# Performance work log

Measured on AMD Instinct MI355X. Metric: run time of the kernel, lower is better.

## Reference

```python
import jax, jax.numpy as jnp
import numpy as np

B, IMG, P, D, E, K, H = 32, 224, 16, 512, 8, 2, 8
G = IMG // P
T = G * G          # 196 patches
PD = P * P         # 256 patch dim
FF = 4 * D         # expert hidden

def _posenc(t, d):
    pos = jnp.arange(t, dtype=jnp.float32)[:, None]
    i = jnp.arange(0, d, 2, dtype=jnp.float32)
    ang = pos / jnp.power(10000.0, i / d)
    pe = jnp.zeros((t, d), jnp.float32)
    pe = pe.at[:, 0::2].set(jnp.sin(ang))
    pe = pe.at[:, 1::2].set(jnp.cos(ang))
    return pe

def _attn(x, Wq, Wk, Wv, Wo, bo):
    bs, t, d = x.shape
    hs = d // H
    q = (x @ Wq).reshape(bs, t, H, hs).transpose(0, 2, 1, 3)
    k = (x @ Wk).reshape(bs, t, H, hs).transpose(0, 2, 1, 3)
    v = (x @ Wv).reshape(bs, t, H, hs).transpose(0, 2, 1, 3)
    wei = jnp.einsum('bhqd,bhkd->bhqk', q, k) * (hs ** -0.5)
    mask = jnp.tril(jnp.ones((t, t), dtype=bool))
    wei = jax.nn.softmax(jnp.where(mask, wei, -jnp.inf), axis=-1)
    o = jnp.einsum('bhqk,bhkd->bhqd', wei, v).transpose(0, 2, 1, 3).reshape(bs, t, d)
    return o @ Wo + bo

def _router(x, Wt, bt, Wn, bn, noise):
    # NoisyTopkRouter: noisy logits, top-k scatter to -inf background, softmax
    logits = x @ Wt + bt
    noisy = logits + noise * jax.nn.softplus(x @ Wn + bn)
    _, topi = jax.lax.top_k(noisy, K)
    sel = jax.nn.one_hot(topi, E, dtype=jnp.float32).sum(-2) > 0  # [B,T,E] bool
    return jax.nn.softmax(jnp.where(sel, noisy, -jnp.inf), axis=-1)

def _moe(x, gate, Wi, bi, Wo, bo):
    # gate is exactly zero off the top-k set, so dense all-expert compute
    # weighted by gate equals the original masked gather/scatter-add combine.
    h = jax.nn.relu(jnp.einsum('btd,edh->bteh', x, Wi) + bi)
    y = jnp.einsum('bteh,ehd->bted', h, Wo) + bo
    return jnp.einsum('bte,bted->btd', gate, y)

def _ln(x, g, b):
    mu = x.mean(-1, keepdims=True)
    var = ((x - mu) ** 2).mean(-1, keepdims=True)
    return (x - mu) / jnp.sqrt(var + 1e-5) * g + b

def _moe_layer(x, pW, pb, Wq, Wk, Wv, Wo, bo, rtW, rtb, rnW, rnb, eWi, ebi, eWo, ebo, lng, lnb, noise):
    x = x @ pW + pb                       # input_projection
    x = _attn(x, Wq, Wk, Wv, Wo, bo)      # multi-head causal self-attention
    gate = _router(x, rtW, rtb, rnW, rnb, noise)
    y = _moe(x, gate, eWi, ebi, eWo, ebo)
    return _ln(y, lng, lnb)               # dropout is identity in eval

def setup_inputs():
    key = jax.random.key(0)
    shapes = {"x": (B, 1, IMG, IMG), "pemb_W": (PD, D), "pemb_b": (D,), "vec_W": (D, D), "vec_b": (D,), "cls_W": (D, D), "cls_b": (D,)}
    for l in ("1", "2"):
        shapes.update({f"p{l}_W": (D, D), f"p{l}_b": (D,), f"Wq{l}": (D, D), f"Wk{l}": (D, D), f"Wv{l}": (D, D), f"Wo{l}": (D, D), f"bo{l}": (D,), f"rt{l}_W": (D, E), f"rt{l}_b": (E,), f"rn{l}_W": (D, E), f"rn{l}_b": (E,), f"eWi{l}": (E, D, FF), f"ebi{l}": (E, FF), f"eWo{l}": (E, FF, D), f"ebo{l}": (E, D), f"ln{l}_g": (D,), f"ln{l}_b": (D,), f"noise{l}": (B, T, E)})
    out = {}
    for i, (name, shp) in enumerate(shapes.items()):
        k = jax.random.fold_in(key, i)
        if name.startswith("ln") and name.endswith("_g"):
            out[name] = jnp.ones(shp, jnp.float32)
        else:
            scale = 1.0 if name == "x" or name.startswith("noise") else 0.02
            out[name] = jax.random.normal(k, shp, jnp.float32) * scale
    return out

def reference(x, pemb_W, pemb_b, vec_W, vec_b, cls_W, cls_b, p1_W, p1_b, Wq1, Wk1, Wv1, Wo1, bo1, rt1_W, rt1_b, rn1_W, rn1_b, eWi1, ebi1, eWo1, ebo1, ln1_g, ln1_b, noise1, p2_W, p2_b, Wq2, Wk2, Wv2, Wo2, bo2, rt2_W, rt2_b, rn2_W, rn2_b, eWi2, ebi2, eWo2, ebo2, ln2_g, ln2_b, noise2):
    bs = x.shape[0]
    # patchify (c==1): [B,1,IMG,IMG] -> [B,T,PD]
    patches = x[:, 0].reshape(bs, G, P, G, P).transpose(0, 1, 3, 2, 4).reshape(bs, T, PD)
    h = patches @ pemb_W + pemb_b + _posenc(T, D)[None]
    f1 = _moe_layer(h, p1_W, p1_b, Wq1, Wk1, Wv1, Wo1, bo1, rt1_W, rt1_b, rn1_W, rn1_b, eWi1, ebi1, eWo1, ebo1, ln1_g, ln1_b, noise1)
    first_vector = f1 @ vec_W + vec_b
    f2 = _moe_layer(first_vector, p2_W, p2_b, Wq2, Wk2, Wv2, Wo2, bo2, rt2_W, rt2_b, rn2_W, rn2_b, eWi2, ebi2, eWo2, ebo2, ln2_g, ln2_b, noise2)
    second_vector = f2 @ vec_W + vec_b
    # source bug: second_attn_weights is None; treated as uniform ones ->
    # mean over dim1 of ones is 1, so global = sum over patches.
    global_vector = second_vector.sum(axis=1)
    cls_vector = global_vector @ cls_W + cls_b
    return first_vector, second_vector, global_vector, cls_vector
```

## Files before the change

### kernel.cpp

```cpp
#include <hip/hip_runtime.h>

#define BT 6272
#define TT 196
#define DM 512
#define FFD 2048
#define NE 8
#define ABUF 3211264
#define SLOTS 12544

typedef float f32x4 __attribute__((ext_vector_type(4)));
typedef __bf16 bf16x8 __attribute__((ext_vector_type(8)));

__device__ __forceinline__ ushort f2bf(float f){
  union { float f; unsigned u; } v; v.f = f;
  unsigned u = v.u;
  u += 0x7fffu + ((u >> 16) & 1u);
  return (ushort)(u >> 16);
}
__device__ __forceinline__ float bf2f(ushort u){
  union { unsigned u; float f; } c; c.u = ((unsigned)u) << 16; return c.f;
}
__device__ __forceinline__ void splitbf(float v, ushort& hi, ushort& lo){
  union { float f; unsigned u; } c; c.f = v;
  hi = (ushort)(c.u >> 16);
  union { unsigned u; float f; } hf; hf.u = c.u & 0xffff0000u;
  lo = f2bf(v - hf.f);
}
__device__ __forceinline__ void glds16(const ushort* g, ushort* l){
  __builtin_amdgcn_global_load_lds(
      (const __attribute__((address_space(1))) unsigned int*)g,
      (__attribute__((address_space(3))) unsigned int*)l, 16, 0, 0);
}

__global__ void patchify_k(const float* __restrict__ x, ushort* __restrict__ oh, ushort* __restrict__ ol){
  int bt = blockIdx.x;
  int t = bt % TT, b = bt / TT;
  int pd = threadIdx.x;
  int g1 = t / 14, g2 = t % 14, p1 = pd >> 4, p2 = pd & 15;
  int src = (b*224 + g1*16 + p1)*224 + g2*16 + p2;
  float v = x[src];
  ushort hu, lu; splitbf(v, hu, lu);
  oh[(size_t)bt*256 + pd] = hu;
  ol[(size_t)bt*256 + pd] = lu;
}

__global__ void posenc_k(float* __restrict__ pe){
  int t = blockIdx.x, c = threadIdx.x;
  int m2 = c & ~1;
  double ang = (double)t * pow(10000.0, -(double)m2 / 512.0);
  double vv = (c & 1) ? cos(ang) : sin(ang);
  pe[t*DM + c] = (float)vv;
}

__global__ __launch_bounds__(256)
void wsplit_k(const float* __restrict__ src, ushort* __restrict__ dh, ushort* __restrict__ dl,
              int R, int C){
  __shared__ float t[32][33];
  int c0 = blockIdx.x << 5, r0 = blockIdx.y << 5;
  int tx = threadIdx.x & 31, ty = threadIdx.x >> 5;
  #pragma unroll
  for (int i = 0; i < 32; i += 8)
    t[ty+i][tx] = src[(size_t)(r0+ty+i)*C + c0 + tx];
  __syncthreads();
  #pragma unroll
  for (int i = 0; i < 32; i += 8){
    float v = t[tx][ty+i];
    ushort hu, lu; splitbf(v, hu, lu);
    dh[(size_t)(c0+ty+i)*R + r0 + tx] = hu;
    dl[(size_t)(c0+ty+i)*R + r0 + tx] = lu;
  }
}

__global__ __launch_bounds__(256)
void wsplit4_k(const float* __restrict__ s0, const float* __restrict__ s1,
               const float* __restrict__ s2, const float* __restrict__ s3,
               ushort* __restrict__ dQkvH, ushort* __restrict__ dQkvL,
               ushort* __restrict__ dWoH, ushort* __restrict__ dWoL)
{
  int z = blockIdx.z;
  const float* src = (z==0)? s0 : (z==1)? s1 : (z==2)? s2 : s3;
  ushort* dh; ushort* dl;
  if (z == 3){ dh = dWoH; dl = dWoL; }
  else { dh = dQkvH + (size_t)z*DM*DM; dl = dQkvL + (size_t)z*DM*DM; }
  __shared__ float t[32][33];
  int c0 = blockIdx.x << 5, r0 = blockIdx.y << 5;
  int tx = threadIdx.x & 31, ty = threadIdx.x >> 5;
  #pragma unroll
  for (int i = 0; i < 32; i += 8)
    t[ty+i][tx] = src[(size_t)(r0+ty+i)*DM + c0 + tx];
  __syncthreads();
  #pragma unroll
  for (int i = 0; i < 32; i += 8){
    float v = t[tx][ty+i];
    ushort hu, lu; splitbf(v, hu, lu);
    dh[(size_t)(c0+ty+i)*DM + r0 + tx] = hu;
    dl[(size_t)(c0+ty+i)*DM + r0 + tx] = lu;
  }
}

__global__ void esplit_k(const float* __restrict__ src, ushort* __restrict__ dh, ushort* __restrict__ dl){
  int i = blockIdx.x*256 + threadIdx.x;
  ushort hu, lu; splitbf(src[i], hu, lu);
  dh[i] = hu; dl[i] = lu;
}

__global__ __launch_bounds__(256)
void bfold_k(const float* __restrict__ pb, const float* __restrict__ Wq,
             const float* __restrict__ Wk, const float* __restrict__ Wv,
             float* __restrict__ bf){
  __shared__ float pbs[DM];
  int tid = threadIdx.x;
  for (int i = tid; i < DM; i += 256) pbs[i] = pb[i];
  __syncthreads();
  int n = blockIdx.x*256 + tid;
  const float* W = (n < 512) ? Wq : (n < 1024) ? Wk : Wv;
  int c = n & 511;
  float s = 0.f;
  for (int d = 0; d < DM; ++d) s += pbs[d] * W[(size_t)d*DM + c];
  bf[n] = s;
}

__global__ __launch_bounds__(256)
void gemm_s(const ushort* __restrict__ Ah, const ushort* __restrict__ Al,
            const ushort* __restrict__ Bh, const ushort* __restrict__ Bl,
            const float* __restrict__ bias, const float* __restrict__ pe,
            float* __restrict__ Cf, ushort* __restrict__ Ch, ushort* __restrict__ Cl,
            int N, int kld)
{
  __shared__ ushort Ahs[128*32];
  __shared__ ushort Als[128*32];
  __shared__ ushort Bhs[128*32];
  __shared__ ushort Bls[128*32];
  int tid = threadIdx.x;
  int row0 = blockIdx.y << 7, col0 = blockIdx.x << 7;
  int lane = tid & 63, w = tid >> 6;
  int wr = w >> 1, wc = w & 1;
  int fr = lane & 15, fu = lane >> 4;
  int srow = 16*w + (lane >> 2);
  int cs = ((lane & 3) ^ ((srow >> 1) & 3)) << 3;
  const ushort* gAh0 = Ah + (size_t)(row0 + srow) * kld + cs;
  const ushort* gAh1 = Ah + (size_t)(row0 + 64 + srow) * kld + cs;
  const ushort* gAl0 = Al + (size_t)(row0 + srow) * kld + cs;
  const ushort* gAl1 = Al + (size_t)(row0 + 64 + srow) * kld + cs;
  const ushort* gBh0 = Bh + (size_t)(col0 + srow) * kld + cs;
  const ushort* gBh1 = Bh + (size_t)(col0 + 64 + srow) * kld + cs;
  const ushort* gBl0 = Bl + (size_t)(col0 + srow) * kld + cs;
  const ushort* gBl1 = Bl + (size_t)(col0 + 64 + srow) * kld + cs;
  ushort* lAh0 = &Ahs[(16*w)*32];      ushort* lAh1 = &Ahs[(64+16*w)*32];
  ushort* lAl0 = &Als[(16*w)*32];      ushort* lAl1 = &Als[(64+16*w)*32];
  ushort* lBh0 = &Bhs[(16*w)*32];      ushort* lBh1 = &Bhs[(64+16*w)*32];
  ushort* lBl0 = &Bls[(16*w)*32];      ushort* lBl1 = &Bls[(64+16*w)*32];
  f32x4 acc[4][4] = {};
  for (int k0 = 0; k0 < kld; k0 += 32){
    __syncthreads();
    glds16(gAh0 + k0, lAh0); glds16(gAh1 + k0, lAh1);
    glds16(gAl0 + k0, lAl0); glds16(gAl1 + k0, lAl1);
    glds16(gBh0 + k0, lBh0); glds16(gBh1 + k0, lBh1);
    glds16(gBl0 + k0, lBl0); glds16(gBl1 + k0, lBl1);
    __syncthreads();
    bf16x8 ah[4], al[4];
    #pragma unroll
    for (int i = 0; i < 4; ++i){
      int Ra = (wr<<6) + (i<<4) + fr;
      int oa = Ra*32 + ((fu ^ ((Ra>>1)&3))<<3);
      ah[i] = *(const bf16x8*)&Ahs[oa];
      al[i] = *(const bf16x8*)&Als[oa];
    }
    #pragma unroll
    for (int j = 0; j < 4; ++j){
      int Rb = (wc<<6) + (j<<4) + fr;
      int ob = Rb*32 + ((fu ^ ((Rb>>1)&3))<<3);
      bf16x8 bh = *(const bf16x8*)&Bhs[ob];
      bf16x8 bl = *(const bf16x8*)&Bls[ob];
      #pragma unroll
      for (int i = 0; i < 4; ++i){
        acc[i][j] = __builtin_amdgcn_mfma_f32_16x16x32_bf16(ah[i], bh, acc[i][j], 0, 0, 0);
        acc[i][j] = __builtin_amdgcn_mfma_f32_16x16x32_bf16(al[i], bh, acc[i][j], 0, 0, 0);
        acc[i][j] = __builtin_amdgcn_mfma_f32_16x16x32_bf16(ah[i], bl, acc[i][j], 0, 0, 0);
      }
    }
  }
  int fq = lane >> 4;
  #pragma unroll
  for (int j = 0; j < 4; ++j){
    int col = col0 + (wc<<6) + (j<<4) + fr;
    float bv = bias ? bias[col] : 0.f;
    #pragma unroll
    for (int i = 0; i < 4; ++i){
      #pragma unroll
      for (int q = 0; q < 4; ++q){
        int rr = row0 + (wr<<6) + (i<<4) + (fq<<2) + q;
        float v = acc[i][j][q] + bv;
        if (pe) v += pe[(size_t)(rr % TT)*DM + col];
        size_t off = (size_t)rr*N + col;
        if (Cf) Cf[off] = v;
        if (Ch){
          ushort hu, lu; splitbf(v, hu, lu);
          Ch[off] = hu; Cl[off] = lu;
        }
      }
    }
  }
}

__global__ __launch_bounds__(256)
void gemm_f32(const float* __restrict__ A, const float* __restrict__ Bw,
              float* __restrict__ C, const float* __restrict__ bias,
              float* __restrict__ obf, int M, int N, int K)
{
  __shared__ float As[16][68];
  __shared__ float Bs[16][68];
  int tid = threadIdx.x;
  int row0 = blockIdx.y << 6, col0 = blockIdx.x << 6;
  int ar = tid >> 2, ak = (tid & 3) << 2;
  int bk = tid >> 4, bn = (tid & 15) << 2;
  int n0 = (tid & 15) << 2, m0 = (tid >> 4) << 2;
  float acc[4][4] = {};
  bool arow_ok = (row0 + ar) < M;
  const float* Aldg = A + (size_t)(row0 + ar) * K + ak;
  const float* Bldg = Bw + (size_t)bk * N + col0 + bn;
  for (int k0 = 0; k0 < K; k0 += 16){
    float4 av = make_float4(0.f,0.f,0.f,0.f);
    if (arow_ok) av = *(const float4*)(Aldg + k0);
    float4 bv = *(const float4*)(Bldg + (size_t)k0 * N);
    __syncthreads();
    As[ak+0][ar]=av.x; As[ak+1][ar]=av.y; As[ak+2][ar]=av.z; As[ak+3][ar]=av.w;
    *(float4*)&Bs[bk][bn] = bv;
    __syncthreads();
    #pragma unroll
    for (int kk = 0; kk < 16; ++kk){
      float4 a = *(const float4*)&As[kk][m0];
      float4 b = *(const float4*)&Bs[kk][n0];
      float aa[4] = {a.x,a.y,a.z,a.w};
      float bb[4] = {b.x,b.y,b.z,b.w};
      #pragma unroll
      for (int i = 0; i < 4; ++i)
        #pragma unroll
        for (int j = 0; j < 4; ++j)
          acc[i][j] += aa[i]*bb[j];
    }
  }
  float4 badd = make_float4(0.f,0.f,0.f,0.f);
  if (bias) badd = *(const float4*)(bias + col0 + n0);
  #pragma unroll
  for (int i = 0; i < 4; ++i){
    int gr = row0 + m0 + i;
    if (gr < M){
      float4 r = make_float4(acc[i][0]+badd.x, acc[i][1]+badd.y, acc[i][2]+badd.z, acc[i][3]+badd.w);
      *(float4*)(C + (size_t)gr*N + col0 + n0) = r;
      if (obf) *(float4*)(obf + (size_t)gr*N + col0 + n0) = r;
    }
  }
}

__global__ __launch_bounds__(256)
void fattn_k(const ushort* __restrict__ Xh, const ushort* __restrict__ Xl,
             ushort* __restrict__ oh, ushort* __restrict__ ol)
{
  __shared__ ushort Kh[64][72], Kl[64][72];
  __shared__ ushort Vth[64][72], Vtl[64][72];
  __shared__ ushort Ph[64][72], Pl[64][72];
  int qt = blockIdx.x, bh = blockIdx.y;
  int b = bh >> 3, h = bh & 7;
  int tid = threadIdx.x;
  int w = tid >> 6, lane = tid & 63;
  int fr = lane & 15, fu = lane >> 4;
  int qrow_f = qt*64 + w*16 + fr;
  int qtok = b*TT + (qrow_f < TT ? qrow_f : TT-1);
  const ushort* qph = Xh + (size_t)qtok*1536 + h*64 + fu*8;
  const ushort* qpl = Xl + (size_t)qtok*1536 + h*64 + fu*8;
  bf16x8 qh0 = *(const bf16x8*)(qph);
  bf16x8 qh1 = *(const bf16x8*)(qph + 32);
  bf16x8 ql0 = *(const bf16x8*)(qpl);
  bf16x8 ql1 = *(const bf16x8*)(qpl + 32);
  f32x4 o_acc[4] = {};
  float m_i[4], l_i[4];
  #pragma unroll
  for (int q = 0; q < 4; ++q){ m_i[q] = -3e38f; l_i[q] = 0.f; }
  int sr = tid >> 2, sc = (tid & 3) << 4;
  int ktiles = qt + 1;
  for (int kt = 0; kt < ktiles; ++kt){
    __syncthreads();
    {
      int jrow = kt*64 + sr;
      int jtok = b*TT + (jrow < TT ? jrow : TT-1);
      const ushort* kph = Xh + (size_t)jtok*1536 + 512 + h*64 + sc;
      const ushort* kpl = Xl + (size_t)jtok*1536 + 512 + h*64 + sc;
      *(uint4*)&Kh[sr][sc]   = *(const uint4*)kph;
      *(uint4*)&Kh[sr][sc+8] = *(const uint4*)(kph + 8);
      *(uint4*)&Kl[sr][sc]   = *(const uint4*)kpl;
      *(uint4*)&Kl[sr][sc+8] = *(const uint4*)(kpl + 8);
      const ushort* vph = Xh + (size_t)jtok*1536 + 1024 + h*64 + sc;
      const ushort* vpl = Xl + (size_t)jtok*1536 + 1024 + h*64 + sc;
      ushort tv[16];
      *(uint4*)&tv[0] = *(const uint4*)vph;
      *(uint4*)&tv[8] = *(const uint4*)(vph + 8);
      #pragma unroll
      for (int t = 0; t < 16; ++t) Vth[sc + t][sr] = tv[t];
      *(uint4*)&tv[0] = *(const uint4*)vpl;
      *(uint4*)&tv[8] = *(const uint4*)(vpl + 8);
      #pragma unroll
      for (int t = 0; t < 16; ++t) Vtl[sc + t][sr] = tv[t];
    }
    __syncthreads();
    f32x4 sacc[4] = {};
    #pragma unroll
    for (int j = 0; j < 4; ++j){
      bf16x8 kh0 = *(const bf16x8*)&Kh[j*16 + fr][fu*8];
      bf16x8 kh1 = *(const bf16x8*)&Kh[j*16 + fr][32 + fu*8];
      bf16x8 kl0 = *(const bf16x8*)&Kl[j*16 + fr][fu*8];
      bf16x8 kl1 = *(const bf16x8*)&Kl[j*16 + fr][32 + fu*8];
      sacc[j] = __builtin_amdgcn_mfma_f32_16x16x32_bf16(qh0, kh0, sacc[j], 0, 0, 0);
      sacc[j] = __builtin_amdgcn_mfma_f32_16x16x32_bf16(ql0, kh0, sacc[j], 0, 0, 0);
      sacc[j] = __builtin_amdgcn_mfma_f32_16x16x32_bf16(qh0, kl0, sacc[j], 0, 0, 0);
      sacc[j] = __builtin_amdgcn_mfma_f32_16x16x32_bf16(qh1, kh1, sacc[j], 0, 0, 0);
      sacc[j] = __builtin_amdgcn_mfma_f32_16x16x32_bf16(ql1, kh1, sacc[j], 0, 0, 0);
      sacc[j] = __builtin_amdgcn_mfma_f32_16x16x32_bf16(qh1, kl1, sacc[j], 0, 0, 0);
    }
    int rbase = qt*64 + w*16 + (fu<<2);
    int cg = kt*64 + fr;
    float p[4][4];
    #pragma unroll
    for (int q = 0; q < 4; ++q){
      int rg = rbase + q;
      float sv[4];
      #pragma unroll
      for (int j = 0; j < 4; ++j){
        int cj = cg + j*16;
        sv[j] = (cj <= rg && cj < TT) ? sacc[j][q]*0.125f : -3e38f;
      }
      float mx = fmaxf(fmaxf(sv[0],sv[1]), fmaxf(sv[2],sv[3]));
      #pragma unroll
      for (int off = 1; off < 16; off <<= 1) mx = fmaxf(mx, __shfl_xor(mx, off, 64));
      float mnew = fmaxf(m_i[q], mx);
      float al = expf(m_i[q] - mnew);
      l_i[q] *= al;
      o_acc[0][q] *= al; o_acc[1][q] *= al; o_acc[2][q] *= al; o_acc[3][q] *= al;
      float ps = 0.f;
      #pragma unroll
      for (int j = 0; j < 4; ++j){ p[q][j] = expf(sv[j] - mnew); ps += p[q][j]; }
      #pragma unroll
      for (int off = 1; off < 16; off <<= 1) ps += __shfl_xor(ps, off, 64);
      l_i[q] += ps;
      m_i[q] = mnew;
    }
    #pragma unroll
    for (int q = 0; q < 4; ++q){
      int pr = w*16 + (fu<<2) + q;
      #pragma unroll
      for (int j = 0; j < 4; ++j){
        ushort hu, lu; splitbf(p[q][j], hu, lu);
        Ph[pr][j*16 + fr] = hu;
        Pl[pr][j*16 + fr] = lu;
      }
    }
    bf16x8 ph0 = *(const bf16x8*)&Ph[w*16 + fr][fu*8];
    bf16x8 ph1 = *(const bf16x8*)&Ph[w*16 + fr][32 + fu*8];
    bf16x8 pl0 = *(const bf16x8*)&Pl[w*16 + fr][fu*8];
    bf16x8 pl1 = *(const bf16x8*)&Pl[w*16 + fr][32 + fu*8];
    #pragma unroll
    for (int jd = 0; jd < 4; ++jd){
      bf16x8 vh0 = *(const bf16x8*)&Vth[jd*16 + fr][fu*8];
      bf16x8 vh1 = *(const bf16x8*)&Vth[jd*16 + fr][32 + fu*8];
      bf16x8 vl0 = *(const bf16x8*)&Vtl[jd*16 + fr][fu*8];
      bf16x8 vl1 = *(const bf16x8*)&Vtl[jd*16 + fr][32 + fu*8];
      o_acc[jd] = __builtin_amdgcn_mfma_f32_16x16x32_bf16(ph0, vh0, o_acc[jd], 0, 0, 0);
      o_acc[jd] = __builtin_amdgcn_mfma_f32_16x16x32_bf16(pl0, vh0, o_acc[jd], 0, 0, 0);
      o_acc[jd] = __builtin_amdgcn_mfma_f32_16x16x32_bf16(ph0, vl0, o_acc[jd], 0, 0, 0);
      o_acc[jd] = __builtin_amdgcn_mfma_f32_16x16x32_bf16(ph1, vh1, o_acc[jd], 0, 0, 0);
      o_acc[jd] = __builtin_amdgcn_mfma_f32_16x16x32_bf16(pl1, vh1, o_acc[jd], 0, 0, 0);
      o_acc[jd] = __builtin_amdgcn_mfma_f32_16x16x32_bf16(ph1, vl1, o_acc[jd], 0, 0, 0);
    }
  }
  #pragma unroll
  for (int q = 0; q < 4; ++q){
    int rg = qt*64 + w*16 + (fu<<2) + q;
    if (rg < TT){
      float inv = 1.f / l_i[q];
      size_t rowoff = (size_t)(b*TT + rg)*DM + h*64 + fr;
      #pragma unroll
      for (int jd = 0; jd < 4; ++jd){
        float v = o_acc[jd][q] * inv;
        ushort hu, lu; splitbf(v, hu, lu);
        oh[rowoff + jd*16] = hu;
        ol[rowoff + jd*16] = lu;
      }
    }
  }
}

__global__ __launch_bounds__(256)
void router2_k(const ushort* __restrict__ Xh, const ushort* __restrict__ Xl,
               const float* __restrict__ rtW, const float* __restrict__ rtb,
               const float* __restrict__ rnW, const float* __restrict__ rnb, const float* __restrict__ nz,
               int* __restrict__ tok_e, float* __restrict__ tok_g)
{
  __shared__ float Wt[8*513];
  __shared__ float Wn[8*513];
  int tid = threadIdx.x;
  for (int i = tid*4; i < DM*8; i += 1024){
    float4 t = *(const float4*)(rtW + i);
    float4 n = *(const float4*)(rnW + i);
    int d = i >> 3, e = i & 7;
    Wt[(e+0)*513 + d] = t.x; Wt[(e+1)*513 + d] = t.y; Wt[(e+2)*513 + d] = t.z; Wt[(e+3)*513 + d] = t.w;
    Wn[(e+0)*513 + d] = n.x; Wn[(e+1)*513 + d] = n.y; Wn[(e+2)*513 + d] = n.z; Wn[(e+3)*513 + d] = n.w;
  }
  __syncthreads();
  int w = tid >> 6, lane = tid & 63;
  int t = (blockIdx.x << 2) + w;
  const ushort* xh = Xh + (size_t)t * DM;
  const ushort* xl = Xl + (size_t)t * DM;
  float at[8] = {}, an[8] = {};
  #pragma unroll
  for (int u = 0; u < 8; ++u){
    int d = (u<<6) + lane;
    float xv = bf2f(xh[d]) + bf2f(xl[d]);
    #pragma unroll
    for (int e = 0; e < 8; ++e){
      at[e] += xv * Wt[e*513 + d];
      an[e] += xv * Wn[e*513 + d];
    }
  }
  #pragma unroll
  for (int off = 32; off; off >>= 1){
    #pragma unroll
    for (int e = 0; e < 8; ++e){
      at[e] += __shfl_xor(at[e], off, 64);
      an[e] += __shfl_xor(an[e], off, 64);
    }
  }
  if (lane == 0){
    float ns[8];
    #pragma unroll
    for (int e = 0; e < 8; ++e){
      float lt = at[e] + rtb[e];
      float ln_ = an[e] + rnb[e];
      float sp = (ln_ > 0.f) ? (ln_ + log1pf(expf(-ln_))) : log1pf(expf(ln_));
      ns[e] = lt + nz[(size_t)t*8 + e] * sp;
    }
    int i1 = 0; float n1 = ns[0];
    #pragma unroll
    for (int e = 1; e < 8; ++e) if (ns[e] > n1){ n1 = ns[e]; i1 = e; }
    int i2 = -1; float n2 = -3e38f;
    #pragma unroll
    for (int e = 0; e < 8; ++e) if (e != i1 && ns[e] > n2){ n2 = ns[e]; i2 = e; }
    float ex = expf(n2 - n1);
    float inv = 1.f / (1.f + ex);
    tok_e[t*2]   = i1; tok_g[t*2]   = inv;
    tok_e[t*2+1] = i2; tok_g[t*2+1] = ex * inv;
  }
}

__global__ __launch_bounds__(1024)
void route_assign_k(const int* __restrict__ tok_e, int* __restrict__ offs_g,
                    int* __restrict__ idx_c, int* __restrict__ tok_slot)
{
  __shared__ int hist[NE];
  __shared__ int cur[NE];
  int tid = threadIdx.x;
  if (tid < NE) hist[tid] = 0;
  __syncthreads();
  for (int i = tid; i < BT*2; i += 1024) atomicAdd(&hist[tok_e[i]], 1);
  __syncthreads();
  if (tid == 0){
    int s = 0;
    for (int e = 0; e < NE; ++e){ offs_g[e] = s; cur[e] = s; s += hist[e]; }
    offs_g[NE] = s;
  }
  __syncthreads();
  for (int i = tid; i < BT*2; i += 1024){
    int e = tok_e[i];
    int p = atomicAdd(&cur[e], 1);
    idx_c[p] = i >> 1;
    tok_slot[i] = p;
  }
}

__global__ __launch_bounds__(256)
void transconv_k(const float* __restrict__ src, ushort* __restrict__ dst, int R, int C){
  __shared__ float t[32][33];
  int e = blockIdx.z;
  src += (size_t)e * R * C;
  dst += (size_t)e * R * C;
  int c0 = blockIdx.x << 5, r0 = blockIdx.y << 5;
  int tx = threadIdx.x & 31, ty = threadIdx.x >> 5;
  #pragma unroll
  for (int i = 0; i < 32; i += 8)
    t[ty+i][tx] = src[(size_t)(r0+ty+i)*C + c0 + tx];
  __syncthreads();
  #pragma unroll
  for (int i = 0; i < 32; i += 8)
    dst[(size_t)(c0+ty+i)*R + r0 + tx] = f2bf(t[tx][ty+i]);
}

__global__ void gatherconv_k(const ushort* __restrict__ Xh, const int* __restrict__ idx,
                             ushort* __restrict__ Xg){
  int s = blockIdx.x;
  const ushort* xp = Xh + (size_t)idx[s] * DM;
  ushort* op = Xg + (size_t)s * DM;
  int i = threadIdx.x * 2;
  *(ushort2*)(op + i) = *(const ushort2*)(xp + i);
}

template<int MODE>
__global__ __launch_bounds__(256)
void moe_mfma(const ushort* __restrict__ A, const ushort* __restrict__ Bt,
              const float* __restrict__ bias, const int* __restrict__ offs,
              void* __restrict__ Out, int kld, int ldb, int out_ld, int accum)
{
  int e = blockIdx.z;
  int base = offs[e], cnt = offs[e+1] - base;
  int row0 = blockIdx.y << 7;
  if (row0 >= cnt) return;
  int col0 = blockIdx.x << 7;
  __shared__ ushort As[128*32];
  __shared__ ushort Bs[128*32];
  int tid = threadIdx.x, lane = tid & 63, w = tid >> 6;
  int wr = w >> 1, wc = w & 1;
  int fr = lane & 15, fu = lane >> 4;
  int srow = 16*w + (lane >> 2);
  int cs = ((lane & 3) ^ ((srow >> 1) & 3)) << 3;
  int ar0 = base + row0 + srow;      if (ar0 > SLOTS-1) ar0 = SLOTS-1;
  int ar1 = base + row0 + 64 + srow; if (ar1 > SLOTS-1) ar1 = SLOTS-1;
  const ushort* gA0 = A + (size_t)ar0 * kld + cs;
  const ushort* gA1 = A + (size_t)ar1 * kld + cs;
  const ushort* Bb = Bt + (size_t)e * ((size_t)FFD*DM);
  const ushort* gB0 = Bb + (size_t)(col0 + srow) * ldb + cs;
  const ushort* gB1 = Bb + (size_t)(col0 + 64 + srow) * ldb + cs;
  ushort* lA0 = &As[(16*w)*32];  ushort* lA1 = &As[(64+16*w)*32];
  ushort* lB0 = &Bs[(16*w)*32];  ushort* lB1 = &Bs[(64+16*w)*32];
  f32x4 acc[4][4] = {};
  for (int k0 = 0; k0 < kld; k0 += 32){
    __syncthreads();
    glds16(gA0 + k0, lA0);
    glds16(gA1 + k0, lA1);
    glds16(gB0 + k0, lB0);
    glds16(gB1 + k0, lB1);
    __syncthreads();
    bf16x8 af[4], bf[4];
    #pragma unroll
    for (int i = 0; i < 4; ++i){
      int Ra = (wr<<6) + (i<<4) + fr;
      af[i] = *(const bf16x8*)&As[Ra*32 + ((fu ^ ((Ra>>1)&3))<<3)];
      int Rb = (wc<<6) + (i<<4) + fr;
      bf[i] = *(const bf16x8*)&Bs[Rb*32 + ((fu ^ ((Rb>>1)&3))<<3)];
    }
    #pragma unroll
    for (int i = 0; i < 4; ++i)
      #pragma unroll
      for (int j = 0; j < 4; ++j)
        acc[i][j] = __builtin_amdgcn_mfma_f32_16x16x32_bf16(af[i], bf[j], acc[i][j], 0, 0, 0);
  }
  int fq = lane >> 4;
  #pragma unroll
  for (int j = 0; j < 4; ++j){
    int col = col0 + (wc<<6) + (j<<4) + fr;
    float bv = bias[(size_t)e * ((MODE==0)?FFD:DM) + col];
    #pragma unroll
    for (int i = 0; i < 4; ++i){
      #pragma unroll
      for (int q = 0; q < 4; ++q){
        int rr = row0 + (wr<<6) + (i<<4) + (fq<<2) + q;
        if (rr < cnt){
          if (MODE == 0){
            float vv = acc[i][j][q] + bv;
            ((ushort*)Out)[(size_t)(base+rr)*out_ld + col] = f2bf(fmaxf(vv, 0.f));
          } else {
            float* yp = (float*)Out + (size_t)(base+rr)*out_ld + col;
            *yp = acc[i][j][q] + (accum ? *yp : bv);
          }
        }
      }
    }
  }
}

__global__ __launch_bounds__(256)
void combine_ln_k(const float* __restrict__ Ye, const int* __restrict__ tok_slot,
                  const float* __restrict__ tok_g, const float* __restrict__ g,
                  const float* __restrict__ bb, ushort* __restrict__ oh, ushort* __restrict__ ol)
{
  int t = blockIdx.x, tid = threadIdx.x;
  int s1 = tok_slot[t*2], s2 = tok_slot[t*2+1];
  float g1 = tok_g[t*2], g2 = tok_g[t*2+1];
  const float* y1 = Ye + (size_t)s1*DM;
  const float* y2 = Ye + (size_t)s2*DM;
  float v0 = g1*y1[tid]     + g2*y2[tid];
  float v1 = g1*y1[tid+256] + g2*y2[tid+256];
  __shared__ float red[8];
  int w = tid >> 6, lane = tid & 63;
  float s = v0 + v1;
  #pragma unroll
  for (int off = 32; off; off >>= 1) s += __shfl_xor(s, off, 64);
  if (lane == 0) red[w] = s;
  __syncthreads();
  float mu = (red[0]+red[1]+red[2]+red[3]) * (1.f/512.f);
  float d0 = v0 - mu, d1 = v1 - mu;
  float q2 = d0*d0 + d1*d1;
  #pragma unroll
  for (int off = 32; off; off >>= 1) q2 += __shfl_xor(q2, off, 64);
  if (lane == 0) red[4+w] = q2;
  __syncthreads();
  float var = (red[4]+red[5]+red[6]+red[7]) * (1.f/512.f);
  float r = 1.f / sqrtf(var + 1e-5f);
  float r0v = d0*r*g[tid]     + bb[tid];
  float r1v = d1*r*g[tid+256] + bb[tid+256];
  ushort hu, lu;
  splitbf(r0v, hu, lu);
  oh[(size_t)t*DM + tid] = hu; ol[(size_t)t*DM + tid] = lu;
  splitbf(r1v, hu, lu);
  oh[(size_t)t*DM + tid + 256] = hu; ol[(size_t)t*DM + tid + 256] = lu;
}

__global__ void gsum_k(const float* __restrict__ sv, float* __restrict__ gb, float* __restrict__ gout){
  int i = blockIdx.x*256 + threadIdx.x;
  int b = i >> 9, d = i & 511;
  const float* p = sv + (size_t)b*TT*DM + d;
  float s = 0.f;
  for (int t = 0; t < TT; ++t) s += p[(size_t)t*DM];
  gb[i] = s; gout[i] = s;
}

extern "C" void kernel_launch(void* const* d_in, const int* in_sizes, int n_in,
                              void* d_out, int out_size, void* d_ws, size_t ws_size,
                              hipStream_t stream)
{
  (void)in_sizes; (void)n_in; (void)out_size;
  const float* xin   = (const float*)d_in[0];
  const float* pembW = (const float*)d_in[1];
  const float* pembB = (const float*)d_in[2];
  const float* vecW  = (const float*)d_in[3];
  const float* vecB  = (const float*)d_in[4];
  const float* clsW  = (const float*)d_in[5];
  const float* clsB  = (const float*)d_in[6];
  float* out = (float*)d_out;

  const size_t QKV_SH  = (size_t)2*BT*1536;
  const size_t RMIN_SH = QKV_SH + (size_t)2*1536*DM + (size_t)2*DM*DM;
  const size_t FIXF =
      (size_t)SLOTS*DM
    + (size_t)2*ABUF
    + (size_t)SLOTS*DM/2
    + (size_t)NE*FFD*DM
    + (size_t)256*DM
    + (size_t)DM*DM
    + (size_t)3*DM*DM
    + (size_t)DM*DM
    + (size_t)TT*DM + 2048
    + 16384*2 + SLOTS + SLOTS*3 + 64;
  int fcw = 256;
  for (int cand = 2048; cand >= 256; cand >>= 1){
    size_t reg_sh = (size_t)SLOTS*cand > RMIN_SH ? (size_t)SLOTS*cand : RMIN_SH;
    size_t need = (FIXF + reg_sh/2) * sizeof(float);
    if (need <= ws_size){ fcw = cand; break; }
  }
  size_t region_sh = (size_t)SLOTS*fcw > RMIN_SH ? (size_t)SLOTS*fcw : RMIN_SH;

  float* ws = (float*)d_ws;
  float* Yexp = ws;
  ushort* S0h = (ushort*)(Yexp + (size_t)SLOTS*DM);
  ushort* S0l = S0h + ABUF;
  ushort* S1h = S0l + ABUF;
  ushort* S1l = S1h + ABUF;
  ushort* region = S1l + ABUF;
  ushort* Xg   = region + region_sh;
  ushort* WiT  = Xg + (size_t)SLOTS*DM;
  ushort* WoT  = WiT + (size_t)NE*FFD*DM;
  ushort* PembH = WoT + (size_t)NE*FFD*DM;
  ushort* PembL = PembH + 256*DM;
  ushort* VecH = PembL + 256*DM;
  ushort* VecL = VecH + DM*DM;
  ushort* QkvWH = VecL + DM*DM;
  ushort* QkvWL = QkvWH + 3*DM*DM;
  ushort* WoSH = QkvWL + 3*DM*DM;
  ushort* WoSL = WoSH + DM*DM;
  float* pe    = (float*)(WoSL + DM*DM);
  float* bfold = pe + TT*DM;
  float* gbv   = bfold + 2048;
  float* clsbuf= gbv + 16384;
  float* tok_g = clsbuf + 16384;
  int* tok_e   = (int*)(tok_g + SLOTS);
  int* tok_slot= tok_e + SLOTS;
  int* idx_c   = tok_slot + SLOTS;
  int* offs    = idx_c + SLOTS;
  ushort* QKVh = region;
  ushort* QKVl = region + (size_t)BT*1536;
  ushort* FoldWH = region + QKV_SH;
  ushort* FoldWL = FoldWH + (size_t)1536*DM;
  ushort* PWh  = FoldWL + (size_t)1536*DM;
  ushort* PWl  = PWh + (size_t)DM*DM;
  ushort* H1b  = region;
  ushort* PATh = region;
  ushort* PATl = region + (size_t)BT*256;

  patchify_k<<<dim3(BT), dim3(256), 0, stream>>>(xin, PATh, PATl);
  posenc_k<<<dim3(TT), dim3(512), 0, stream>>>(pe);
  wsplit_k<<<dim3(16, 8), dim3(256), 0, stream>>>(pembW, PembH, PembL, 256, DM);
  wsplit_k<<<dim3(16, 16), dim3(256), 0, stream>>>(vecW, VecH, VecL, DM, DM);
  gemm_s<<<dim3(4,49), dim3(256), 0, stream>>>(PATh, PATl, PembH, PembL, pembB, pe,
                                               nullptr, S0h, S0l, DM, 256);

  ushort *INh = S0h, *INl = S0l, *TPh = S1h, *TPl = S1l;
  for (int l = 0; l < 2; ++l){
    int base = 7 + 18*l;
    const float* pW  = (const float*)d_in[base+0];
    const float* pb  = (const float*)d_in[base+1];
    const float* Wq  = (const float*)d_in[base+2];
    const float* Wk  = (const float*)d_in[base+3];
    const float* Wv  = (const float*)d_in[base+4];
    const float* Wo  = (const float*)d_in[base+5];
    const float* bo  = (const float*)d_in[base+6];
    const float* rtW = (const float*)d_in[base+7];
    const float* rtb = (const float*)d_in[base+8];
    const float* rnW = (const float*)d_in[base+9];
    const float* rnb = (const float*)d_in[base+10];
    const float* eWi = (const float*)d_in[base+11];
    const float* ebi = (const float*)d_in[base+12];
    const float* eWo = (const float*)d_in[base+13];
    const float* ebo = (const float*)d_in[base+14];
    const float* lng = (const float*)d_in[base+15];
    const float* lnb = (const float*)d_in[base+16];
    const float* nz  = (const float*)d_in[base+17];

    wsplit4_k<<<dim3(16,16,4), dim3(256), 0, stream>>>(Wq, Wk, Wv, Wo,
                                                       QkvWH, QkvWL, WoSH, WoSL);
    esplit_k<<<dim3(1024), dim3(256), 0, stream>>>(pW, PWh, PWl);
    gemm_s<<<dim3(4,12), dim3(256), 0, stream>>>(QkvWH, QkvWL, PWh, PWl, nullptr, nullptr,
                                                 nullptr, FoldWH, FoldWL, DM, DM);
    bfold_k<<<dim3(6), dim3(256), 0, stream>>>(pb, Wq, Wk, Wv, bfold);
    gemm_s<<<dim3(12,49), dim3(256), 0, stream>>>(INh, INl, FoldWH, FoldWL, bfold, nullptr,
                                                 nullptr, QKVh, QKVl, 1536, DM);
    fattn_k<<<dim3(4,256), dim3(256), 0, stream>>>(QKVh, QKVl, INh, INl);
    gemm_s<<<dim3(4,49), dim3(256), 0, stream>>>(INh, INl, WoSH, WoSL, bo, nullptr,
                                                 nullptr, TPh, TPl, DM, DM);
    transconv_k<<<dim3(FFD/32, DM/32, NE), dim3(256), 0, stream>>>(eWi, WiT, DM, FFD);
    transconv_k<<<dim3(DM/32, FFD/32, NE), dim3(256), 0, stream>>>(eWo, WoT, FFD, DM);
    router2_k<<<dim3(BT/4), dim3(256), 0, stream>>>(TPh, TPl, rtW, rtb, rnW, rnb, nz, tok_e, tok_g);
    route_assign_k<<<dim3(1), dim3(1024), 0, stream>>>(tok_e, offs, idx_c, tok_slot);
    gatherconv_k<<<dim3(SLOTS), dim3(256), 0, stream>>>(TPh, idx_c, Xg);
    for (int c0 = 0; c0 < FFD; c0 += fcw){
      moe_mfma<0><<<dim3(fcw/128, 49, NE), dim3(256), 0, stream>>>(
          Xg, WiT + (size_t)c0*DM, ebi + c0, offs, (void*)H1b, DM, DM, fcw, 0);
      moe_mfma<1><<<dim3(DM/128, 49, NE), dim3(256), 0, stream>>>(
          H1b, WoT + c0, ebo, offs, (void*)Yexp, fcw, FFD, DM, c0);
    }
    combine_ln_k<<<dim3(BT), dim3(256), 0, stream>>>(Yexp, tok_slot, tok_g, lng, lnb, INh, INl);
    gemm_s<<<dim3(4,49), dim3(256), 0, stream>>>(INh, INl, VecH, VecL, vecB, nullptr,
                                                 out + (size_t)l*ABUF, TPh, TPl, DM, DM);
    ushort* th = INh; INh = TPh; TPh = th;
    ushort* tl = INl; INl = TPl; TPl = tl;
  }

  gsum_k<<<dim3(64), dim3(256), 0, stream>>>(out + ABUF, gbv, out + 2*ABUF);
  gemm_f32<<<dim3(8,1), dim3(256), 0, stream>>>(gbv, clsW, clsbuf, clsB, out + 2*ABUF + 16384, 32, DM, DM);
}
```

Measured before the change: 1.141 ms.

## Double-buffer LDS tiles in GEMM kernels and parallelize bias folding

The gemm_s and moe_mfma kernels now keep two LDS tile buffers. Each iteration prefetches the next k-tile into the idle buffer while MFMAs run on the current one, which drops one barrier per iteration and overlaps global loads with compute. bfold_k now uses one wavefront per output column with a shuffle reduction across 384 blocks, replacing 6 blocks of serial loops. The cost is doubled LDS usage per block, which may lower occupancy, especially for gemm_s at 64KB.

```diff
diff --git a/kernel.cpp b/kernel.cpp
--- a/kernel.cpp
+++ b/kernel.cpp
@@ -108,16 +108,20 @@
 void bfold_k(const float* __restrict__ pb, const float* __restrict__ Wq,
              const float* __restrict__ Wk, const float* __restrict__ Wv,
              float* __restrict__ bf){
-  __shared__ float pbs[DM];
   int tid = threadIdx.x;
-  for (int i = tid; i < DM; i += 256) pbs[i] = pb[i];
-  __syncthreads();
-  int n = blockIdx.x*256 + tid;
+  int w = tid >> 6, lane = tid & 63;
+  int n = blockIdx.x*4 + w;
   const float* W = (n < 512) ? Wq : (n < 1024) ? Wk : Wv;
   int c = n & 511;
   float s = 0.f;
-  for (int d = 0; d < DM; ++d) s += pbs[d] * W[(size_t)d*DM + c];
-  bf[n] = s;
+  #pragma unroll
+  for (int u = 0; u < 8; ++u){
+    int d = (u<<6) + lane;
+    s += pb[d] * W[(size_t)d*DM + c];
+  }
+  #pragma unroll
+  for (int off = 32; off; off >>= 1) s += __shfl_xor(s, off, 64);
+  if (lane == 0) bf[n] = s;
 }
 
 __global__ __launch_bounds__(256)
@@ -127,10 +131,10 @@
             float* __restrict__ Cf, ushort* __restrict__ Ch, ushort* __restrict__ Cl,
             int N, int kld)
 {
-  __shared__ ushort Ahs[128*32];
-  __shared__ ushort Als[128*32];
-  __shared__ ushort Bhs[128*32];
-  __shared__ ushort Bls[128*32];
+  __shared__ ushort Ahs[2*128*32];
+  __shared__ ushort Als[2*128*32];
+  __shared__ ushort Bhs[2*128*32];
+  __shared__ ushort Bls[2*128*32];
   int tid = threadIdx.x;
   int row0 = blockIdx.y << 7, col0 = blockIdx.x << 7;
   int lane = tid & 63, w = tid >> 6;
@@ -146,30 +150,35 @@
   const ushort* gBh1 = Bh + (size_t)(col0 + 64 + srow) * kld + cs;
   const ushort* gBl0 = Bl + (size_t)(col0 + srow) * kld + cs;
   const ushort* gBl1 = Bl + (size_t)(col0 + 64 + srow) * kld + cs;
-  ushort* lAh0 = &Ahs[(16*w)*32];      ushort* lAh1 = &Ahs[(64+16*w)*32];
-  ushort* lAl0 = &Als[(16*w)*32];      ushort* lAl1 = &Als[(64+16*w)*32];
-  ushort* lBh0 = &Bhs[(16*w)*32];      ushort* lBh1 = &Bhs[(64+16*w)*32];
-  ushort* lBl0 = &Bls[(16*w)*32];      ushort* lBl1 = &Bls[(64+16*w)*32];
+  int lo0 = (16*w)*32, lo1 = (64+16*w)*32;
+  glds16(gAh0, &Ahs[lo0]); glds16(gAh1, &Ahs[lo1]);
+  glds16(gAl0, &Als[lo0]); glds16(gAl1, &Als[lo1]);
+  glds16(gBh0, &Bhs[lo0]); glds16(gBh1, &Bhs[lo1]);
+  glds16(gBl0, &Bls[lo0]); glds16(gBl1, &Bls[lo1]);
   f32x4 acc[4][4] = {};
+  int cur = 0;
   for (int k0 = 0; k0 < kld; k0 += 32){
     __syncthreads();
-    glds16(gAh0 + k0, lAh0); glds16(gAh1 + k0, lAh1);
-    glds16(gAl0 + k0, lAl0); glds16(gAl1 + k0, lAl1);
-    glds16(gBh0 + k0, lBh0); glds16(gBh1 + k0, lBh1);
-    glds16(gBl0 + k0, lBl0); glds16(gBl1 + k0, lBl1);
-    __syncthreads();
+    if (k0 + 32 < kld){
+      int nb = (cur ^ 1) * (128*32);
+      glds16(gAh0 + k0+32, &Ahs[nb+lo0]); glds16(gAh1 + k0+32, &Ahs[nb+lo1]);
+      glds16(gAl0 + k0+32, &Als[nb+lo0]); glds16(gAl1 + k0+32, &Als[nb+lo1]);
+      glds16(gBh0 + k0+32, &Bhs[nb+lo0]); glds16(gBh1 + k0+32, &Bhs[nb+lo1]);
+      glds16(gBl0 + k0+32, &Bls[nb+lo0]); glds16(gBl1 + k0+32, &Bls[nb+lo1]);
+    }
+    int cb = cur * (128*32);
     bf16x8 ah[4], al[4];
     #pragma unroll
     for (int i = 0; i < 4; ++i){
       int Ra = (wr<<6) + (i<<4) + fr;
-      int oa = Ra*32 + ((fu ^ ((Ra>>1)&3))<<3);
+      int oa = cb + Ra*32 + ((fu ^ ((Ra>>1)&3))<<3);
       ah[i] = *(const bf16x8*)&Ahs[oa];
       al[i] = *(const bf16x8*)&Als[oa];
     }
     #pragma unroll
     for (int j = 0; j < 4; ++j){
       int Rb = (wc<<6) + (j<<4) + fr;
-      int ob = Rb*32 + ((fu ^ ((Rb>>1)&3))<<3);
+      int ob = cb + Rb*32 + ((fu ^ ((Rb>>1)&3))<<3);
       bf16x8 bh = *(const bf16x8*)&Bhs[ob];
       bf16x8 bl = *(const bf16x8*)&Bls[ob];
       #pragma unroll
@@ -179,6 +188,7 @@
         acc[i][j] = __builtin_amdgcn_mfma_f32_16x16x32_bf16(ah[i], bl, acc[i][j], 0, 0, 0);
       }
     }
+    cur ^= 1;
   }
   int fq = lane >> 4;
   #pragma unroll
@@ -513,8 +523,8 @@
   int row0 = blockIdx.y << 7;
   if (row0 >= cnt) return;
   int col0 = blockIdx.x << 7;
-  __shared__ ushort As[128*32];
-  __shared__ ushort Bs[128*32];
+  __shared__ ushort As[2*128*32];
+  __shared__ ushort Bs[2*128*32];
   int tid = threadIdx.x, lane = tid & 63, w = tid >> 6;
   int wr = w >> 1, wc = w & 1;
   int fr = lane & 15, fu = lane >> 4;
@@ -527,29 +537,33 @@
   const ushort* Bb = Bt + (size_t)e * ((size_t)FFD*DM);
   const ushort* gB0 = Bb + (size_t)(col0 + srow) * ldb + cs;
   const ushort* gB1 = Bb + (size_t)(col0 + 64 + srow) * ldb + cs;
-  ushort* lA0 = &As[(16*w)*32];  ushort* lA1 = &As[(64+16*w)*32];
-  ushort* lB0 = &Bs[(16*w)*32];  ushort* lB1 = &Bs[(64+16*w)*32];
+  int lo0 = (16*w)*32, lo1 = (64+16*w)*32;
+  glds16(gA0, &As[lo0]); glds16(gA1, &As[lo1]);
+  glds16(gB0, &Bs[lo0]); glds16(gB1, &Bs[lo1]);
   f32x4 acc[4][4] = {};
+  int cur = 0;
   for (int k0 = 0; k0 < kld; k0 += 32){
     __syncthreads();
-    glds16(gA0 + k0, lA0);
-    glds16(gA1 + k0, lA1);
-    glds16(gB0 + k0, lB0);
-    glds16(gB1 + k0, lB1);
-    __syncthreads();
+    if (k0 + 32 < kld){
+      int nb = (cur ^ 1) * (128*32);
+      glds16(gA0 + k0+32, &As[nb+lo0]); glds16(gA1 + k0+32, &As[nb+lo1]);
+      glds16(gB0 + k0+32, &Bs[nb+lo0]); glds16(gB1 + k0+32, &Bs[nb+lo1]);
+    }
+    int cb = cur * (128*32);
     bf16x8 af[4], bf[4];
     #pragma unroll
     for (int i = 0; i < 4; ++i){
       int Ra = (wr<<6) + (i<<4) + fr;
-      af[i] = *(const bf16x8*)&As[Ra*32 + ((fu ^ ((Ra>>1)&3))<<3)];
+      af[i] = *(const bf16x8*)&As[cb + Ra*32 + ((fu ^ ((Ra>>1)&3))<<3)];
       int Rb = (wc<<6) + (i<<4) + fr;
-      bf[i] = *(const bf16x8*)&Bs[Rb*32 + ((fu ^ ((Rb>>1)&3))<<3)];
+      bf[i] = *(const bf16x8*)&Bs[cb + Rb*32 + ((fu ^ ((Rb>>1)&3))<<3)];
     }
     #pragma unroll
     for (int i = 0; i < 4; ++i)
       #pragma unroll
       for (int j = 0; j < 4; ++j)
         acc[i][j] = __builtin_amdgcn_mfma_f32_16x16x32_bf16(af[i], bf[j], acc[i][j], 0, 0, 0);
+    cur ^= 1;
   }
   int fq = lane >> 4;
   #pragma unroll
@@ -727,7 +741,7 @@
     esplit_k<<<dim3(1024), dim3(256), 0, stream>>>(pW, PWh, PWl);
     gemm_s<<<dim3(4,12), dim3(256), 0, stream>>>(QkvWH, QkvWL, PWh, PWl, nullptr, nullptr,
                                                  nullptr, FoldWH, FoldWL, DM, DM);
-    bfold_k<<<dim3(6), dim3(256), 0, stream>>>(pb, Wq, Wk, Wv, bfold);
+    bfold_k<<<dim3(384), dim3(256), 0, stream>>>(pb, Wq, Wk, Wv, bfold);
     gemm_s<<<dim3(12,49), dim3(256), 0, stream>>>(INh, INl, FoldWH, FoldWL, bfold, nullptr,
                                                  nullptr, QKVh, QKVl, 1536, DM);
     fattn_k<<<dim3(4,256), dim3(256), 0, stream>>>(QKVh, QKVl, INh, INl);
```

Measured after the change: 1.091 ms. 4.4% less time.
